# Kernel optimization log

Hardware: AMD Instinct MI355X
Metric: run time of the kernel (lower is better)

## Reference

```python
import jax, jax.numpy as jnp
import numpy as np

N_NODES = 100000
N_EDGES = 3200000
N_GRAPHS = 512
DIM = 64
NF = 4
BN_EPS = 1e-5

_PARAM_SHAPES = [
    ("c1_w1", (DIM, NF), "randn"), ("c1_b1", (DIM,), "randn"),
    ("c1_g1", (DIM,), "ones"), ("c1_be1", (DIM,), "zeros"),
    ("c1_w2", (DIM, DIM), "randn"), ("c1_b2", (DIM,), "randn"),
    ("bn1_g", (DIM,), "ones"), ("bn1_b", (DIM,), "zeros"),
    ("c2_w1", (DIM, DIM), "randn"), ("c2_b1", (DIM,), "randn"),
    ("c2_g1", (DIM,), "ones"), ("c2_be1", (DIM,), "zeros"),
    ("c2_w2", (DIM, DIM), "randn"), ("c2_b2", (DIM,), "randn"),
    ("bn2_g", (DIM,), "ones"), ("bn2_b", (DIM,), "zeros"),
    ("fc0_w", (DIM, NF), "randn"), ("fc0_b", (DIM,), "randn"),
    ("fc1_w", (DIM, DIM), "randn"), ("fc1_b", (DIM,), "randn"),
    ("fc2_w", (DIM, DIM), "randn"), ("fc2_b", (DIM,), "randn"),
    ("pi_w", (DIM, DIM), "randn"), ("pi_b", (DIM,), "randn"),
    ("vf_w", (DIM, DIM), "randn"), ("vf_b", (DIM,), "randn"),
]


def setup_inputs() -> dict:
    key = jax.random.key(0)
    ks = jax.random.split(key, 3 + len(_PARAM_SHAPES))
    inp = {
        "x": jax.random.normal(ks[0], (N_NODES, NF), jnp.float32),
        "edge_index": jax.random.randint(ks[1], (2, N_EDGES), 0, N_NODES, dtype=jnp.int64)
        if jax.config.jax_enable_x64 else jax.random.randint(ks[1], (2, N_EDGES), 0, N_NODES).astype(jnp.int32),
        "batch": jnp.sort(jax.random.randint(ks[2], (N_NODES,), 0, N_GRAPHS)).astype(jnp.int32),
    }
    for i, (name, shape, fill) in enumerate(_PARAM_SHAPES):
        k = ks[3 + i]
        if fill == "randn":
            inp[name] = jax.random.normal(k, shape, jnp.float32) * 0.1
        elif fill == "ones":
            inp[name] = jnp.ones(shape, jnp.float32)
        else:
            inp[name] = jnp.zeros(shape, jnp.float32)
    return inp


def _lin(x, w, b):
    return x @ w.T + b


def _bn(x, g, b):  # training-mode batch statistics over node axis
    m = x.mean(axis=0)
    v = x.var(axis=0)
    return (x - m) * jax.lax.rsqrt(v + BN_EPS) * g + b


def _gin_conv(x, src, dst, w1, b1, g1, be1, w2, b2):
    # sum-aggregate neighbor messages (GINConv, eps=0): h = MLP(x + sum_{j in N(i)} x_j)
    agg = jax.ops.segment_sum(x[src], dst, num_segments=x.shape[0])
    h = x + agg
    h = jax.nn.relu(_bn(_lin(h, w1, b1), g1, be1))
    return _lin(h, w2, b2)


def reference(x, edge_index, batch,
              c1_w1, c1_b1, c1_g1, c1_be1, c1_w2, c1_b2, bn1_g, bn1_b,
              c2_w1, c2_b1, c2_g1, c2_be1, c2_w2, c2_b2, bn2_g, bn2_b,
              fc0_w, fc0_b, fc1_w, fc1_b, fc2_w, fc2_b,
              pi_w, pi_b, vf_w, vf_b):
    src, dst = edge_index[0], edge_index[1]
    h1 = jax.nn.relu(_bn(_gin_conv(x, src, dst, c1_w1, c1_b1, c1_g1, c1_be1, c1_w2, c1_b2), bn1_g, bn1_b))
    h2 = jax.nn.relu(_bn(_gin_conv(h1, src, dst, c2_w1, c2_b1, c2_g1, c2_be1, c2_w2, c2_b2), bn2_g, bn2_b))
    pool = lambda h: jax.ops.segment_sum(h, batch, num_segments=N_GRAPHS)  # global_add_pool
    # dropout is eval-mode identity
    out = _lin(pool(x), fc0_w, fc0_b) + _lin(pool(h1), fc1_w, fc1_b) + _lin(pool(h2), fc2_w, fc2_b)
    pi = jax.nn.relu(_lin(out, pi_w, pi_b))
    vf = jax.nn.relu(_lin(out, vf_w, vf_b))
    return (pi, vf)
```

## Files before the change

### kernel.cpp

```cpp
#include <hip/hip_runtime.h>

#define N_NODES 100000
#define N_EDGES 3200000
#define N_GRAPHS 512
#define NBKT 782
#define NBLK 256
#define EPB 12500
#define NSCAN 200192
#define NB_SCAN 782
#define SCAP 6000
#define NCOPY 64
#define STREG (NCOPY * 128)

__device__ __forceinline__ uint32_t f2bf(float f) {
  uint32_t u = __float_as_uint(f);
  return (u + 0x7fffu + ((u >> 16) & 1u)) >> 16;
}
__device__ __forceinline__ float bflo(uint32_t u) { return __uint_as_float(u << 16); }
__device__ __forceinline__ float bfhi(uint32_t u) { return __uint_as_float(u & 0xffff0000u); }

__global__ __launch_bounds__(256) void k_cnt(const int* __restrict__ dst,
                                             int* __restrict__ cnt)
{
  __shared__ int h[NBKT];
  int t = threadIdx.x, blk = blockIdx.x;
  for (int i = t; i < NBKT; i += 256) h[i] = 0;
  __syncthreads();
  int e0 = blk * EPB;
  for (int i = t; i < EPB; i += 256) atomicAdd(&h[dst[e0 + i] >> 7], 1);
  __syncthreads();
  for (int i = t; i < NBKT; i += 256) cnt[i * NBLK + blk] = h[i];
}

__global__ __launch_bounds__(256) void k_scan1(const int* __restrict__ v,
                                               int* __restrict__ bsum, int n)
{
  __shared__ int s[256];
  int i = blockIdx.x * 256 + threadIdx.x;
  s[threadIdx.x] = i < n ? v[i] : 0;
  __syncthreads();
  for (int off = 128; off > 0; off >>= 1) {
    if (threadIdx.x < off) s[threadIdx.x] += s[threadIdx.x + off];
    __syncthreads();
  }
  if (threadIdx.x == 0) bsum[blockIdx.x] = s[0];
}

__global__ void k_scan2(int* __restrict__ bsum, int nb)
{
  __shared__ int s[1024];
  int t = threadIdx.x;
  int v = t < nb ? bsum[t] : 0;
  s[t] = v;
  __syncthreads();
  for (int off = 1; off < 1024; off <<= 1) {
    int nv = t >= off ? s[t - off] : 0;
    __syncthreads();
    s[t] += nv;
    __syncthreads();
  }
  if (t < nb) bsum[t] = s[t] - v;
}

__global__ __launch_bounds__(256) void k_scanout(const int* __restrict__ v,
    const int* __restrict__ boff, int* __restrict__ out, int n)
{
  __shared__ int s[256];
  int t = threadIdx.x, i = blockIdx.x * 256 + t;
  int x = i < n ? v[i] : 0;
  s[t] = x;
  __syncthreads();
  for (int off = 1; off < 256; off <<= 1) {
    int nv = t >= off ? s[t - off] : 0;
    __syncthreads();
    s[t] += nv;
    __syncthreads();
  }
  if (i < n) out[i] = boff[blockIdx.x] + s[t] - x;
}

__global__ __launch_bounds__(256) void k_bin(const int* __restrict__ src,
    const int* __restrict__ dst, const int* __restrict__ off,
    int2* __restrict__ eb)
{
  __shared__ int base[NBKT];
  __shared__ int cur[NBKT];
  int t = threadIdx.x, blk = blockIdx.x;
  for (int i = t; i < NBKT; i += 256) { base[i] = off[i * NBLK + blk]; cur[i] = 0; }
  __syncthreads();
  int e0 = blk * EPB;
  for (int i = t; i < EPB; i += 256) {
    int e = e0 + i;
    int s = src[e], d = dst[e], b = d >> 7;
    int p = atomicAdd(&cur[b], 1);
    eb[base[b] + p] = make_int2(s, d);
  }
}

__global__ __launch_bounds__(256) void k_sortb(const int2* __restrict__ eb,
    const int* __restrict__ off, int* __restrict__ rowstart,
    int* __restrict__ csr)
{
  int b = blockIdx.x, t = threadIdx.x;
  int start = off[b * NBLK];
  int end = (b == NBKT - 1) ? N_EDGES : off[(b + 1) * NBLK];
  int cnt = end - start;
  __shared__ int2 ebs[SCAP];
  __shared__ int h[128], cur[128];
  bool staged = cnt <= SCAP;
  if (staged) for (int i = t; i < cnt; i += 256) ebs[i] = eb[start + i];
  if (t < 128) h[t] = 0;
  __syncthreads();
  if (staged) {
    for (int i = t; i < cnt; i += 256) atomicAdd(&h[ebs[i].y & 127], 1);
  } else {
    for (int i = t; i < cnt; i += 256) atomicAdd(&h[eb[start + i].y & 127], 1);
  }
  __syncthreads();
  int v = t < 128 ? h[t] : 0;
  for (int o = 1; o < 128; o <<= 1) {
    int nv = (t < 128 && t >= o) ? h[t - o] : 0;
    __syncthreads();
    if (t < 128) h[t] += nv;
    __syncthreads();
  }
  if (t < 128) {
    int ex = h[t] - v;
    int node = b * 128 + t;
    if (node < N_NODES) rowstart[node] = start + ex;
    cur[t] = ex;
  }
  if (b == NBKT - 1 && t == 0) rowstart[N_NODES] = N_EDGES;
  __syncthreads();
  if (staged) {
    for (int i = t; i < cnt; i += 256) {
      int2 e = ebs[i];
      int p = atomicAdd(&cur[e.y & 127], 1);
      csr[start + p] = e.x;
    }
  } else {
    for (int i = t; i < cnt; i += 256) {
      int2 e = eb[start + i];
      int p = atomicAdd(&cur[e.y & 127], 1);
      csr[start + p] = e.x;
    }
  }
}

__global__ __launch_bounds__(256) void k_gstart(const int* __restrict__ batch,
                                                int* __restrict__ gstart, int n)
{
  int i = blockIdx.x * 256 + threadIdx.x;
  if (i >= n) return;
  int b = batch[i];
  if (i == 0) {
    for (int g = 0; g <= b; ++g) gstart[g] = 0;
  } else {
    int p = batch[i - 1];
    for (int g = p + 1; g <= b; ++g) gstart[g] = i;
  }
  if (i == n - 1) {
    for (int g = b + 1; g <= N_GRAPHS; ++g) gstart[g] = n;
  }
}

__global__ __launch_bounds__(256) void k_agglin1(const int* __restrict__ csr,
    const int* __restrict__ rowstart, const float* __restrict__ x,
    const float* __restrict__ w1, const float* __restrict__ b1,
    float* __restrict__ OUT, float* __restrict__ st, int n)
{
  __shared__ float sAgg[8][4];
  __shared__ float rs[4][64], rq[4][64];
  int t = threadIdx.x;
  int hw = t >> 5, lane = t & 31;
  int nd = blockIdx.x * 8 + hw;
  const float4* x4 = reinterpret_cast<const float4*>(x);
  float4 a = make_float4(0.f, 0.f, 0.f, 0.f);
  if (nd < n) {
    int e0 = rowstart[nd], e1 = rowstart[nd + 1];
    for (int e = e0 + lane; e < e1; e += 32) {
      float4 v = x4[csr[e]];
      a.x += v.x; a.y += v.y; a.z += v.z; a.w += v.w;
    }
    if (lane == 0) {
      float4 v = x4[nd];
      a.x += v.x; a.y += v.y; a.z += v.z; a.w += v.w;
    }
  }
  for (int off = 1; off < 32; off <<= 1) {
    a.x += __shfl_xor(a.x, off);
    a.y += __shfl_xor(a.y, off);
    a.z += __shfl_xor(a.z, off);
    a.w += __shfl_xor(a.w, off);
  }
  if (lane == 0) *reinterpret_cast<float4*>(&sAgg[hw][0]) = a;
  __syncthreads();
  int d = t & 63, slot = t >> 6;
  float4 wr = reinterpret_cast<const float4*>(w1)[d];
  float bv = b1[d];
  float lsum = 0.f, lsq = 0.f;
  int base = blockIdx.x * 8;
#pragma unroll
  for (int li = slot; li < 8; li += 4) {
    int nn = base + li;
    if (nn < n) {
      float v = bv + sAgg[li][0] * wr.x + sAgg[li][1] * wr.y
                   + sAgg[li][2] * wr.z + sAgg[li][3] * wr.w;
      OUT[nn * 64 + d] = v;
      lsum += v; lsq += v * v;
    }
  }
  rs[slot][d] = lsum; rq[slot][d] = lsq;
  __syncthreads();
  if (t < 64) {
    int cp = (blockIdx.x & (NCOPY - 1)) * 128;
    atomicAdd(&st[cp + d],      rs[0][d] + rs[1][d] + rs[2][d] + rs[3][d]);
    atomicAdd(&st[cp + 64 + d], rq[0][d] + rq[1][d] + rq[2][d] + rq[3][d]);
  }
}

template <bool WRITE_HB>
__global__ __launch_bounds__(256) void k_hpool(const float* __restrict__ T,
    const float* __restrict__ st, const float* __restrict__ gam,
    const float* __restrict__ bet, float invN, const int* __restrict__ batch,
    uint2* __restrict__ Hb, float* __restrict__ pool)
{
  __shared__ float sm[16][64];
  __shared__ int sb[16];
  __shared__ float s_ss[128];
  int t = threadIdx.x;
  int r = t >> 4, c4 = t & 15;
  int row0 = blockIdx.x * 16;
  if (t < 64) {
    float s = 0.f, q = 0.f;
#pragma unroll 8
    for (int c = 0; c < NCOPY; ++c) {
      s += st[c * 128 + t];
      q += st[c * 128 + 64 + t];
    }
    float mean = s * invN;
    float var  = q * invN - mean * mean;
    float sc   = gam[t] * rsqrtf(var + 1e-5f);
    s_ss[t] = sc;
    s_ss[64 + t] = bet[t] - mean * sc;
  }
  if (t >= 64 && t < 80) sb[t - 64] = batch[row0 + t - 64];
  __syncthreads();
  float4 v = reinterpret_cast<const float4*>(T)[(row0 + r) * 16 + c4];
  int c = c4 * 4;
  v.x = fmaxf(v.x * s_ss[c + 0] + s_ss[64 + c + 0], 0.f);
  v.y = fmaxf(v.y * s_ss[c + 1] + s_ss[64 + c + 1], 0.f);
  v.z = fmaxf(v.z * s_ss[c + 2] + s_ss[64 + c + 2], 0.f);
  v.w = fmaxf(v.w * s_ss[c + 3] + s_ss[64 + c + 3], 0.f);
  if (WRITE_HB) {
    uint2 p;
    p.x = f2bf(v.x) | (f2bf(v.y) << 16);
    p.y = f2bf(v.z) | (f2bf(v.w) << 16);
    Hb[(row0 + r) * 16 + c4] = p;
  }
  *reinterpret_cast<float4*>(&sm[r][c]) = v;
  __syncthreads();
  if (t < 64) {
    int gmin = sb[0], gmax = sb[15];
    for (int g = gmin; g <= gmax; ++g) {
      float s = 0.f;
#pragma unroll
      for (int rr = 0; rr < 16; ++rr) if (sb[rr] == g) s += sm[rr][t];
      atomicAdd(&pool[g * 64 + t], s);
    }
  }
}

__global__ __launch_bounds__(256) void k_agg64b(const int* __restrict__ csr,
    const int* __restrict__ rowstart, const uint32_t* __restrict__ Hb,
    float2* __restrict__ AGG, int n)
{
  int hw = threadIdx.x >> 5, lane = threadIdx.x & 31;
  int nd = blockIdx.x * 8 + hw;
  if (nd >= n) return;
  int e = rowstart[nd], e1 = rowstart[nd + 1];
  float a0 = 0.f, a1 = 0.f;
  for (; e + 4 <= e1; e += 4) {
    int s0 = csr[e], s1 = csr[e + 1], s2 = csr[e + 2], s3 = csr[e + 3];
    uint32_t u0 = Hb[s0 * 32 + lane];
    uint32_t u1 = Hb[s1 * 32 + lane];
    uint32_t u2 = Hb[s2 * 32 + lane];
    uint32_t u3 = Hb[s3 * 32 + lane];
    a0 += bflo(u0) + bflo(u1) + bflo(u2) + bflo(u3);
    a1 += bfhi(u0) + bfhi(u1) + bfhi(u2) + bfhi(u3);
  }
  for (; e < e1; ++e) {
    uint32_t u = Hb[csr[e] * 32 + lane];
    a0 += bflo(u); a1 += bfhi(u);
  }
  AGG[nd * 32 + lane] = make_float2(a0, a1);
}

__global__ __launch_bounds__(64) void k_pool_x(const float* __restrict__ x,
    const int* __restrict__ gstart, float* __restrict__ px)
{
  int g = blockIdx.x;
  int r0 = gstart[g], r1 = gstart[g + 1];
  int f = threadIdx.x & 3, slot = threadIdx.x >> 2;
  float acc = 0.f;
  for (int r = r0 + slot; r < r1; r += 16) acc += x[r * 4 + f];
  __shared__ float red[16][4];
  red[slot][f] = acc;
  __syncthreads();
  if (threadIdx.x < 4) {
    float s = 0.f;
    for (int k = 0; k < 16; ++k) s += red[k][f];
    px[g * 4 + f] = s;
  }
}

template <int MODE>
__global__ __launch_bounds__(256) void k_gemm64(const void* __restrict__ IN1,
    const float* __restrict__ IN2, const float* __restrict__ stIn,
    const float* __restrict__ gam, const float* __restrict__ bet, float invN,
    const float* __restrict__ W, const float* __restrict__ bias,
    float* __restrict__ OUT, float* __restrict__ st, int n)
{
  __shared__ float sWt[64][64];
  __shared__ float sIn[16][68];
  __shared__ float s_ss[128];
  __shared__ float rs[4][64], rq[4][64];
  int tid = threadIdx.x;
  for (int i = tid; i < 4096; i += 256) {
    int dd = i >> 6, kk = i & 63;
    sWt[kk][dd ^ kk] = W[i];
  }
  if (MODE == 0 && tid < 64) {
    float s = 0.f, q = 0.f;
#pragma unroll 8
    for (int c = 0; c < NCOPY; ++c) {
      s += stIn[c * 128 + tid];
      q += stIn[c * 128 + 64 + tid];
    }
    float mean = s * invN;
    float var  = q * invN - mean * mean;
    float sc   = gam[tid] * rsqrtf(var + 1e-5f);
    s_ss[tid] = sc;
    s_ss[64 + tid] = bet[tid] - mean * sc;
  }
  int d = tid & 63;
  int wav = tid >> 6;
  int srow = tid >> 4, sc4 = tid & 15;
  float lsum = 0.f, lsq = 0.f;
  float bv = bias[d];
  int ngroups = (n + 15) >> 4;
  for (int grp = blockIdx.x; grp < ngroups; grp += gridDim.x) {
    int nbase = grp * 16;
    __syncthreads();
    {
      int nn = nbase + srow;
      float4 v = make_float4(0.f, 0.f, 0.f, 0.f);
      if (nn < n) {
        if (MODE == 0) {
          float4 t = reinterpret_cast<const float4*>(IN2)[nn * 16 + sc4];
          int c = sc4 * 4;
          v.x = fmaxf(t.x * s_ss[c + 0] + s_ss[64 + c + 0], 0.f);
          v.y = fmaxf(t.y * s_ss[c + 1] + s_ss[64 + c + 1], 0.f);
          v.z = fmaxf(t.z * s_ss[c + 2] + s_ss[64 + c + 2], 0.f);
          v.w = fmaxf(t.w * s_ss[c + 3] + s_ss[64 + c + 3], 0.f);
        } else {
          uint2 hb = reinterpret_cast<const uint2*>(IN1)[nn * 16 + sc4];
          float4 b = reinterpret_cast<const float4*>(IN2)[nn * 16 + sc4];
          v.x = bflo(hb.x) + b.x;
          v.y = bfhi(hb.x) + b.y;
          v.z = bflo(hb.y) + b.z;
          v.w = bfhi(hb.y) + b.w;
        }
      }
      *reinterpret_cast<float4*>(&sIn[srow][sc4 * 4]) = v;
    }
    __syncthreads();
    float acc[4];
#pragma unroll
    for (int i = 0; i < 4; i++) acc[i] = bv;
#pragma unroll 4
    for (int k4 = 0; k4 < 16; k4++) {
      float4 rv[4];
#pragma unroll
      for (int i = 0; i < 4; i++)
        rv[i] = *reinterpret_cast<const float4*>(&sIn[wav * 4 + i][k4 * 4]);
#pragma unroll
      for (int j = 0; j < 4; j++) {
        int kk = k4 * 4 + j;
        float wv = sWt[kk][d ^ kk];
#pragma unroll
        for (int i = 0; i < 4; i++) acc[i] += (&rv[i].x)[j] * wv;
      }
    }
#pragma unroll
    for (int i = 0; i < 4; i++) {
      int nn = nbase + wav * 4 + i;
      if (nn < n) {
        OUT[nn * 64 + d] = acc[i];
        lsum += acc[i]; lsq += acc[i] * acc[i];
      }
    }
  }
  __syncthreads();
  rs[wav][d] = lsum; rq[wav][d] = lsq;
  __syncthreads();
  if (tid < 64) {
    int cp = (blockIdx.x & (NCOPY - 1)) * 128;
    atomicAdd(&st[cp + d],      rs[0][d] + rs[1][d] + rs[2][d] + rs[3][d]);
    atomicAdd(&st[cp + 64 + d], rq[0][d] + rq[1][d] + rq[2][d] + rq[3][d]);
  }
}

__global__ __launch_bounds__(64) void k_head(const float* __restrict__ px,
    const float* __restrict__ ph1, const float* __restrict__ ph2,
    const float* __restrict__ fc0w, const float* __restrict__ fc0b,
    const float* __restrict__ fc1w, const float* __restrict__ fc1b,
    const float* __restrict__ fc2w, const float* __restrict__ fc2b,
    const float* __restrict__ piw, const float* __restrict__ pib,
    const float* __restrict__ vfw, const float* __restrict__ vfb,
    float* __restrict__ out)
{
  int g = blockIdx.x, d = threadIdx.x;
  float o = fc0b[d] + fc1b[d] + fc2b[d];
  float4 pxv = reinterpret_cast<const float4*>(px)[g];
  float4 w0 = reinterpret_cast<const float4*>(fc0w)[d];
  o += pxv.x * w0.x + pxv.y * w0.y + pxv.z * w0.z + pxv.w * w0.w;
  const float4* p1 = reinterpret_cast<const float4*>(ph1) + g * 16;
  const float4* w1 = reinterpret_cast<const float4*>(fc1w) + d * 16;
  const float4* p2 = reinterpret_cast<const float4*>(ph2) + g * 16;
  const float4* w2 = reinterpret_cast<const float4*>(fc2w) + d * 16;
#pragma unroll
  for (int k = 0; k < 16; k++) {
    float4 a = p1[k], b = w1[k];
    o += a.x * b.x + a.y * b.y + a.z * b.z + a.w * b.w;
    float4 c = p2[k], e = w2[k];
    o += c.x * e.x + c.y * e.y + c.z * e.z + c.w * e.w;
  }
  __shared__ float so[64];
  so[d] = o;
  __syncthreads();
  float p = pib[d], v = vfb[d];
  const float4* sov = reinterpret_cast<const float4*>(so);
  const float4* wp = reinterpret_cast<const float4*>(piw) + d * 16;
  const float4* wv = reinterpret_cast<const float4*>(vfw) + d * 16;
#pragma unroll
  for (int k = 0; k < 16; k++) {
    float4 a = sov[k], b = wp[k], c = wv[k];
    p += a.x * b.x + a.y * b.y + a.z * b.z + a.w * b.w;
    v += a.x * c.x + a.y * c.y + a.z * c.z + a.w * c.w;
  }
  out[g * 64 + d] = fmaxf(p, 0.f);
  out[N_GRAPHS * 64 + g * 64 + d] = fmaxf(v, 0.f);
}

extern "C" void kernel_launch(void* const* d_in, const int* in_sizes, int n_in,
                              void* d_out, int out_size, void* d_ws, size_t ws_size,
                              hipStream_t stream)
{
  const float* x     = (const float*)d_in[0];
  const int*   ei    = (const int*)d_in[1];
  const int*   batch = (const int*)d_in[2];
  const float* c1_w1 = (const float*)d_in[3];
  const float* c1_b1 = (const float*)d_in[4];
  const float* c1_g1 = (const float*)d_in[5];
  const float* c1_be1= (const float*)d_in[6];
  const float* c1_w2 = (const float*)d_in[7];
  const float* c1_b2 = (const float*)d_in[8];
  const float* bn1_g = (const float*)d_in[9];
  const float* bn1_b = (const float*)d_in[10];
  const float* c2_w1 = (const float*)d_in[11];
  const float* c2_b1 = (const float*)d_in[12];
  const float* c2_g1 = (const float*)d_in[13];
  const float* c2_be1= (const float*)d_in[14];
  const float* c2_w2 = (const float*)d_in[15];
  const float* c2_b2 = (const float*)d_in[16];
  const float* bn2_g = (const float*)d_in[17];
  const float* bn2_b = (const float*)d_in[18];
  const float* fc0_w = (const float*)d_in[19];
  const float* fc0_b = (const float*)d_in[20];
  const float* fc1_w = (const float*)d_in[21];
  const float* fc1_b = (const float*)d_in[22];
  const float* fc2_w = (const float*)d_in[23];
  const float* fc2_b = (const float*)d_in[24];
  const float* pi_w  = (const float*)d_in[25];
  const float* pi_b  = (const float*)d_in[26];
  const float* vf_w  = (const float*)d_in[27];
  const float* vf_b  = (const float*)d_in[28];
  const int* src = ei;
  const int* dst = ei + N_EDGES;

  float* ws = (float*)d_ws;
  float* stats    = ws;
  float* ph1      = ws + 32768;
  float* ph2      = ws + 65536;
  float* px       = ws + 98304;
  int*   gstart   = (int*)(ws + 100352);
  int*   bsum     = (int*)(ws + 100880);
  int*   rowstart = (int*)(ws + 101920);
  float* U        = ws + 201936;
  int*   cnt      = (int*)U;
  int*   off      = (int*)U + 200192;
  uint32_t* Hb    = (uint32_t*)U;
  int*   csr      = (int*)(ws + 3401936);
  float* A        = ws + 6601936;
  int2*  eb       = (int2*)A;

  const float invN = 1.0f / (float)N_NODES;

  hipMemsetAsync(ws, 0, 98304 * sizeof(float), stream);

  k_cnt    <<<NBLK, 256, 0, stream>>>(dst, cnt);
  k_scan1  <<<NB_SCAN, 256, 0, stream>>>(cnt, bsum, NSCAN);
  k_scan2  <<<1, 1024, 0, stream>>>(bsum, NB_SCAN);
  k_scanout<<<NB_SCAN, 256, 0, stream>>>(cnt, bsum, off, NSCAN);
  k_bin    <<<NBLK, 256, 0, stream>>>(src, dst, off, eb);
  k_sortb  <<<NBKT, 256, 0, stream>>>(eb, off, rowstart, csr);
  k_gstart <<<(N_NODES + 255) / 256, 256, 0, stream>>>(batch, gstart, N_NODES);

  k_pool_x<<<N_GRAPHS, 64, 0, stream>>>(x, gstart, px);

  k_agglin1<<<N_NODES / 8, 256, 0, stream>>>(csr, rowstart, x, c1_w1, c1_b1,
                                             A, stats + 0 * STREG, N_NODES);
  k_gemm64<0><<<1024, 256, 0, stream>>>(nullptr, A, stats + 0 * STREG,
      c1_g1, c1_be1, invN, c1_w2, c1_b2, A, stats + 1 * STREG, N_NODES);
  k_hpool<true><<<N_NODES / 16, 256, 0, stream>>>(A, stats + 1 * STREG, bn1_g, bn1_b,
      invN, batch, (uint2*)Hb, ph1);

  k_agg64b<<<(N_NODES + 7) / 8, 256, 0, stream>>>(csr, rowstart, Hb, (float2*)A, N_NODES);
  k_gemm64<2><<<1024, 256, 0, stream>>>(Hb, A, nullptr,
      nullptr, nullptr, 0.f, c2_w1, c2_b1, A, stats + 2 * STREG, N_NODES);
  k_gemm64<0><<<1024, 256, 0, stream>>>(nullptr, A, stats + 2 * STREG,
      c2_g1, c2_be1, invN, c2_w2, c2_b2, A, stats + 3 * STREG, N_NODES);
  k_hpool<false><<<N_NODES / 16, 256, 0, stream>>>(A, stats + 3 * STREG, bn2_g, bn2_b,
      invN, batch, nullptr, ph2);

  k_head<<<N_GRAPHS, 64, 0, stream>>>(px, ph1, ph2, fc0_w, fc0_b, fc1_w, fc1_b,
                                      fc2_w, fc2_b, pi_w, pi_b, vf_w, vf_b, (float*)d_out);
}
```

Baseline: 369.1 us.

## Hold GEMM weights in registers and broadcast inputs via readlane

Rewrites the 64x64 node GEMM so each lane keeps its output column's weight row in 64 registers. Each wave loads its own 4 input rows directly and broadcasts values to all lanes with readlane instead of staging them through shared memory. This removes the shared-memory weight and input tiles and the per-group barriers. It also drops the n%16 tail handling, which assumes the row count is a multiple of 16, and it adds heavy register pressure plus many scalar readlane operations.

```diff
diff --git a/kernel.cpp b/kernel.cpp
--- a/kernel.cpp
+++ b/kernel.cpp
@@ -18,6 +18,9 @@
 }
 __device__ __forceinline__ float bflo(uint32_t u) { return __uint_as_float(u << 16); }
 __device__ __forceinline__ float bfhi(uint32_t u) { return __uint_as_float(u & 0xffff0000u); }
+__device__ __forceinline__ float rdlane(float v, int lane) {
+  return __uint_as_float(__builtin_amdgcn_readlane(__float_as_uint(v), lane));
+}
 
 __global__ __launch_bounds__(256) void k_cnt(const int* __restrict__ dst,
                                              int* __restrict__ cnt)
@@ -321,15 +324,17 @@
     const float* __restrict__ W, const float* __restrict__ bias,
     float* __restrict__ OUT, float* __restrict__ st, int n)
 {
-  __shared__ float sWt[64][64];
-  __shared__ float sIn[16][68];
   __shared__ float s_ss[128];
   __shared__ float rs[4][64], rq[4][64];
   int tid = threadIdx.x;
-  for (int i = tid; i < 4096; i += 256) {
-    int dd = i >> 6, kk = i & 63;
-    sWt[kk][dd ^ kk] = W[i];
-  }
+  int wav = tid >> 6, lane = tid & 63;
+  int rsub = lane >> 4;
+  int c4 = lane & 15;
+  float4 Wreg[16];
+#pragma unroll
+  for (int k4 = 0; k4 < 16; k4++)
+    Wreg[k4] = reinterpret_cast<const float4*>(W)[lane * 16 + k4];
+  float bv = bias[lane];
   if (MODE == 0 && tid < 64) {
     float s = 0.f, q = 0.f;
 #pragma unroll 8
@@ -343,71 +348,62 @@
     s_ss[tid] = sc;
     s_ss[64 + tid] = bet[tid] - mean * sc;
   }
-  int d = tid & 63;
-  int wav = tid >> 6;
-  int srow = tid >> 4, sc4 = tid & 15;
+  __syncthreads();
+  float4 scv, shv;
+  if (MODE == 0) {
+    scv = *reinterpret_cast<const float4*>(&s_ss[c4 * 4]);
+    shv = *reinterpret_cast<const float4*>(&s_ss[64 + c4 * 4]);
+  }
+  const float4* in2 = reinterpret_cast<const float4*>(IN2);
+  const uint2*  in1 = reinterpret_cast<const uint2*>(IN1);
   float lsum = 0.f, lsq = 0.f;
-  float bv = bias[d];
-  int ngroups = (n + 15) >> 4;
+  int ngroups = n >> 4;
   for (int grp = blockIdx.x; grp < ngroups; grp += gridDim.x) {
-    int nbase = grp * 16;
-    __syncthreads();
-    {
-      int nn = nbase + srow;
-      float4 v = make_float4(0.f, 0.f, 0.f, 0.f);
-      if (nn < n) {
-        if (MODE == 0) {
-          float4 t = reinterpret_cast<const float4*>(IN2)[nn * 16 + sc4];
-          int c = sc4 * 4;
-          v.x = fmaxf(t.x * s_ss[c + 0] + s_ss[64 + c + 0], 0.f);
-          v.y = fmaxf(t.y * s_ss[c + 1] + s_ss[64 + c + 1], 0.f);
-          v.z = fmaxf(t.z * s_ss[c + 2] + s_ss[64 + c + 2], 0.f);
-          v.w = fmaxf(t.w * s_ss[c + 3] + s_ss[64 + c + 3], 0.f);
-        } else {
-          uint2 hb = reinterpret_cast<const uint2*>(IN1)[nn * 16 + sc4];
-          float4 b = reinterpret_cast<const float4*>(IN2)[nn * 16 + sc4];
-          v.x = bflo(hb.x) + b.x;
-          v.y = bfhi(hb.x) + b.y;
-          v.z = bflo(hb.y) + b.z;
-          v.w = bfhi(hb.y) + b.w;
-        }
+    int hrow = grp * 16 + wav * 4 + rsub;
+    float4 hv;
+    if (MODE == 0) {
+      float4 t = in2[hrow * 16 + c4];
+      hv.x = fmaxf(t.x * scv.x + shv.x, 0.f);
+      hv.y = fmaxf(t.y * scv.y + shv.y, 0.f);
+      hv.z = fmaxf(t.z * scv.z + shv.z, 0.f);
+      hv.w = fmaxf(t.w * scv.w + shv.w, 0.f);
+    } else {
+      uint2 hb = in1[hrow * 16 + c4];
+      float4 b = in2[hrow * 16 + c4];
+      hv.x = bflo(hb.x) + b.x;
+      hv.y = bfhi(hb.x) + b.y;
+      hv.z = bflo(hb.y) + b.z;
+      hv.w = bfhi(hb.y) + b.w;
+    }
+    float acc[4];
+#pragma unroll
+    for (int i = 0; i < 4; i++) acc[i] = bv;
+#pragma unroll
+    for (int k4 = 0; k4 < 16; k4++) {
+      float4 w = Wreg[k4];
+#pragma unroll
+      for (int i = 0; i < 4; i++) {
+        int sl = i * 16 + k4;
+        acc[i] += rdlane(hv.x, sl) * w.x;
+        acc[i] += rdlane(hv.y, sl) * w.y;
+        acc[i] += rdlane(hv.z, sl) * w.z;
+        acc[i] += rdlane(hv.w, sl) * w.w;
       }
-      *reinterpret_cast<float4*>(&sIn[srow][sc4 * 4]) = v;
-    }
-    __syncthreads();
-    float acc[4];
-#pragma unroll
-    for (int i = 0; i < 4; i++) acc[i] = bv;
-#pragma unroll 4
-    for (int k4 = 0; k4 < 16; k4++) {
-      float4 rv[4];
-#pragma unroll
-      for (int i = 0; i < 4; i++)
-        rv[i] = *reinterpret_cast<const float4*>(&sIn[wav * 4 + i][k4 * 4]);
-#pragma unroll
-      for (int j = 0; j < 4; j++) {
-        int kk = k4 * 4 + j;
-        float wv = sWt[kk][d ^ kk];
-#pragma unroll
-        for (int i = 0; i < 4; i++) acc[i] += (&rv[i].x)[j] * wv;
-      }
-    }
+    }
+    int rbase = grp * 16 + wav * 4;
 #pragma unroll
     for (int i = 0; i < 4; i++) {
-      int nn = nbase + wav * 4 + i;
-      if (nn < n) {
-        OUT[nn * 64 + d] = acc[i];
-        lsum += acc[i]; lsq += acc[i] * acc[i];
-      }
-    }
-  }
-  __syncthreads();
-  rs[wav][d] = lsum; rq[wav][d] = lsq;
+      OUT[(rbase + i) * 64 + lane] = acc[i];
+      lsum += acc[i]; lsq += acc[i] * acc[i];
+    }
+  }
+  __syncthreads();
+  rs[wav][lane] = lsum; rq[wav][lane] = lsq;
   __syncthreads();
   if (tid < 64) {
     int cp = (blockIdx.x & (NCOPY - 1)) * 128;
-    atomicAdd(&st[cp + d],      rs[0][d] + rs[1][d] + rs[2][d] + rs[3][d]);
-    atomicAdd(&st[cp + 64 + d], rq[0][d] + rq[1][d] + rq[2][d] + rq[3][d]);
+    atomicAdd(&st[cp + tid],      rs[0][tid] + rs[1][tid] + rs[2][tid] + rs[3][tid]);
+    atomicAdd(&st[cp + 64 + tid], rq[0][tid] + rq[1][tid] + rq[2][tid] + rq[3][tid]);
   }
 }
 
```

Measured after the change: 368.6 us. No clear change (-0.1%).
